# Kernel optimization log

Measured on AMD Instinct MI355X. Metric: run time of the kernel, lower is better.

The kernel has to match this reference:

```python
import jax, jax.numpy as jnp
import numpy as np

N = 27          # n_agents
NA = 33         # n_actions
OFF = 6         # semantic_action_offset
ATK = NA - OFF  # 27 attack actions
HID = 256       # rnn_hidden_dim
HEADS = 4
HD = 16         # head_dim
V = 8           # comm_value_dim
REL = 5
TOPK = 4
IN = 322
FLAT = HEADS * V  # 32
FUSE_SCALE = 0.1
GATE_FLOOR = 0.0
NEG = -1e10


def setup_inputs() -> dict:
    key = jax.random.key(0)
    ks = iter(jax.random.split(key, 40))
    r = lambda *s: jax.random.normal(next(ks), s, dtype=jnp.float32) * 0.05
    BS = 1024
    inp = {
        'inputs': jax.random.normal(next(ks), (BS * N, IN), dtype=jnp.float32),
        'hidden_state': jax.random.normal(next(ks), (BS * N, HID), dtype=jnp.float32),
        'relation_features': jax.random.normal(next(ks), (BS, N, N, REL), dtype=jnp.float32),
        'W1': r(HID, IN), 'b1': r(HID),
        'Wih': r(3 * HID, HID), 'bih': r(3 * HID),
        'Whh': r(3 * HID, HID), 'bhh': r(3 * HID),
        'Wp1': r(HID, HID), 'bp1': r(HID),
        'Wp2': r(NA, HID), 'bp2': r(NA),
        'Wq': r(HEADS * HD, HID), 'bq': r(HEADS * HD),
        'Wk': r(HEADS * HD, HID + REL), 'bk': r(HEADS * HD),
        'Wv': r(HEADS * V, ATK + 2), 'bv': r(HEADS * V),
        'ln_g': jnp.ones((FLAT,), jnp.float32), 'ln_b': jnp.zeros((FLAT,), jnp.float32),
        'Wg1': r(HID, HID + FLAT), 'bg1': r(HID),
        'Wg2': r(1, HID), 'bg2': jnp.full((1,), -2.5, jnp.float32),  # attack_gate_init_bias
        'Wd1': r(HID, HID + FLAT), 'bd1': r(HID),
        'Wd2': r(ATK, HID) * 0.2, 'bd2': r(ATK) * 0.2,  # small random instead of zero-init for nontrivial test
        'null_key': r(HEADS, HD), 'null_value': r(HEADS, V),
        'bs': BS,
    }
    return inp


def _topk_mask(scores, k):
    # scores: [bs, N, N+1, HEADS]; keep top-k along axis 2
    st = jnp.moveaxis(scores, 2, -1)                # [bs, N, HEADS, N+1]
    thr = jax.lax.top_k(st, k)[0][..., -1:]
    st = jnp.where(st >= thr, st, NEG)
    return jnp.moveaxis(st, -1, 2)


def _forward(inputs, hidden_state, relation_features, W1, b1, Wih, bih, Whh, bhh,
             Wp1, bp1, Wp2, bp2, Wq, bq, Wk, bk, Wv, bv, ln_g, ln_b,
             Wg1, bg1, Wg2, bg2, Wd1, bd1, Wd2, bd2, null_key, null_value, bs):
    x = jax.nn.relu(inputs @ W1.T + b1)
    h_in = hidden_state.reshape(-1, HID)
    # PyTorch GRUCell
    gi = x @ Wih.T + bih
    gh = h_in @ Whh.T + bhh
    ir, iz, inn = jnp.split(gi, 3, axis=-1)
    hr, hz, hn = jnp.split(gh, 3, axis=-1)
    rg = jax.nn.sigmoid(ir + hr)
    zg = jax.nn.sigmoid(iz + hz)
    ng = jnp.tanh(inn + rg * hn)
    h = (1.0 - zg) * ng + zg * h_in

    ah = h.reshape(bs, N, HID)                       # agent_hidden
    logits = jax.nn.relu(ah @ Wp1.T + bp1) @ Wp2.T + bp2   # [bs,N,NA]
    base_logits = logits[:, :, :OFF]
    attack_logits = logits[:, :, OFF:]

    # intent features (avail_actions=None path)
    attack_probs = jax.nn.softmax(attack_logits, axis=-1)
    top1 = jnp.max(attack_probs, axis=-1, keepdims=True)
    can_attack = jnp.ones((bs, N, 1), attack_probs.dtype)
    value_source = jnp.concatenate([attack_probs, can_attack, top1], axis=-1)
    sender_values = (value_source @ Wv.T + bv).reshape(bs, N, HEADS, V)

    queries = (ah @ Wq.T + bq).reshape(bs, N, HEADS, HD)
    # Linear over concat([sender_hidden, relation]) == split-weight sum
    Wk_h, Wk_r = Wk[:, :HID], Wk[:, HID:]
    key_h = ah @ Wk_h.T                              # [bs, N(send), A]
    key_r = jnp.einsum('bijr,ar->bija', relation_features, Wk_r)
    pair_keys = (key_h[:, None, :, :] + key_r + bk).reshape(bs, N, N, HEADS, HD)

    scale = 1.0 / np.sqrt(HD)
    scores = jnp.einsum('bihd,bijhd->bijh', queries, pair_keys) * scale
    eye = jnp.eye(N, dtype=bool)[None, :, :, None]
    scores = jnp.where(eye, NEG, scores)
    null_scores = jnp.einsum('bihd,hd->bih', queries, null_key)[:, :, None, :] * scale
    scores = jnp.concatenate([scores, null_scores], axis=2)   # [bs,N,N+1,HEADS]

    alpha = jax.nn.softmax(_topk_mask(scores, TOPK), axis=2)
    messages = (jnp.einsum('bijh,bjhv->bihv', alpha[:, :, :N], sender_values)
                + alpha[:, :, N, :, None] * null_value)        # [bs,N,HEADS,V]
    flat = messages.reshape(bs, N, FLAT)
    mu = jnp.mean(flat, axis=-1, keepdims=True)
    var = jnp.var(flat, axis=-1, keepdims=True)
    normed = (flat - mu) * jax.lax.rsqrt(var + 1e-5) * ln_g + ln_b

    fusion = jnp.concatenate([ah, normed], axis=-1)
    raw_gate = jax.nn.sigmoid(jax.nn.relu(fusion @ Wg1.T + bg1) @ Wg2.T + bg2)
    gate = GATE_FLOOR + (1.0 - GATE_FLOOR) * raw_gate
    delta = jax.nn.relu(fusion @ Wd1.T + bd1) @ Wd2.T + bd2
    fused = attack_logits + FUSE_SCALE * gate * delta
    final = jnp.concatenate([base_logits, fused], axis=-1).reshape(bs * N, NA)
    return final, h


def reference(inputs, hidden_state, relation_features, W1, b1, Wih, bih, Whh, bhh,
              Wp1, bp1, Wp2, bp2, Wq, bq, Wk, bk, Wv, bv, ln_g, ln_b,
              Wg1, bg1, Wg2, bg2, Wd1, bd1, Wd2, bd2, null_key, null_value, bs):
    return _forward(inputs, hidden_state, relation_features, W1, b1, Wih, bih, Whh, bhh,
                    Wp1, bp1, Wp2, bp2, Wq, bq, Wk, bk, Wv, bv, ln_g, ln_b,
                    Wg1, bg1, Wg2, bg2, Wd1, bd1, Wd2, bd2, null_key, null_value, bs)
```

## Files before the change

### kernel.cpp

```cpp
#include <hip/hip_runtime.h>
#include <cstdint>
#include <cstddef>

#define ROWS 27648
#define NEGV (-1e10f)

typedef __attribute__((ext_vector_type(8))) short bf16x8;
typedef __attribute__((ext_vector_type(4))) short short4v;
typedef __attribute__((ext_vector_type(4))) float f32x4;

__device__ __forceinline__ float sigmoidf_(float x) { return 1.f / (1.f + __expf(-x)); }
__device__ __forceinline__ float bf2f(short s) {
  union { float f; unsigned u; } x; x.u = ((unsigned)(unsigned short)s) << 16; return x.f;
}
__device__ __forceinline__ short f2bf(float f) {
  union { float f; unsigned u; } x; x.f = f;
  unsigned r = (x.u + 0x7fffu + ((x.u >> 16) & 1u)) >> 16;
  return (short)r;
}

#define GLDS(gp, lp) __builtin_amdgcn_global_load_lds( \
  (const __attribute__((address_space(1))) void*)(gp), \
  (__attribute__((address_space(3))) void*)(lp), 16, 0, 0)

template <int ACT, int BF16OUT>
__global__ __launch_bounds__(256) void gemm_mfma(
    const short* __restrict__ A, int lda,
    const short* __restrict__ B, int ldb,
    const float* __restrict__ bias,
    void* __restrict__ Cv, int ldc, int nstore, int K) {
  extern __shared__ short smem[];
  short* As = smem;
  short* Bs = smem + 8192;
  const int tid = threadIdx.x;
  const int wave = tid >> 6, lane = tid & 63;
  const int m0 = blockIdx.x * 128, n0 = blockIdx.y * 128;
  const int srow = lane >> 3;
  const int scol = ((lane & 7) ^ srow) * 8;
  const int sr0 = wave * 32;
  const int wm = (wave >> 1) * 64, wn = (wave & 1) * 64;
  const int fr = lane & 15, fk = (lane >> 4) * 8;

  f32x4 acc[4][4] = {};

  const short* pA = A + (size_t)(m0 + sr0 + srow) * lda + scol;
  const short* pB = B + (size_t)(n0 + sr0 + srow) * ldb + scol;
  short* lA = &As[sr0 * 64];
  short* lB = &Bs[sr0 * 64];

  const int KB = K & ~63;
  for (int k0 = 0; k0 < KB; k0 += 64) {
#pragma unroll
    for (int g = 0; g < 4; ++g) {
      GLDS(pA + k0 + g * 8 * lda, lA + g * 512);
      GLDS(pB + k0 + g * 8 * ldb, lB + g * 512);
    }
    __syncthreads();
#pragma unroll
    for (int ks = 0; ks < 2; ++ks) {
      bf16x8 af[4], bfr[4];
#pragma unroll
      for (int t = 0; t < 4; ++t) {
        const int ra = wm + t * 16 + fr;
        const int rb = wn + t * 16 + fr;
        af[t]  = *(const bf16x8*)&As[(ra * 64 + ks * 32 + fk) ^ ((ra & 7) << 3)];
        bfr[t] = *(const bf16x8*)&Bs[(rb * 64 + ks * 32 + fk) ^ ((rb & 7) << 3)];
      }
#pragma unroll
      for (int i = 0; i < 4; ++i)
#pragma unroll
        for (int j = 0; j < 4; ++j)
          acc[i][j] = __builtin_amdgcn_mfma_f32_16x16x32_bf16(af[i], bfr[j], acc[i][j], 0, 0, 0);
    }
    __syncthreads();
  }

  if (K & 32) {
    short* As2 = smem + 16384;
    short* Bs2 = smem + 20480;
    const int sr2 = lane >> 2, sc2 = (lane & 3) * 8;
    const short* qA = A + (size_t)(m0 + sr0 + sr2) * lda + sc2 + KB;
    const short* qB = B + (size_t)(n0 + sr0 + sr2) * ldb + sc2 + KB;
    GLDS(qA, &As2[sr0 * 32]);
    GLDS(qA + 16 * lda, &As2[(sr0 + 16) * 32]);
    GLDS(qB, &Bs2[sr0 * 32]);
    GLDS(qB + 16 * ldb, &Bs2[(sr0 + 16) * 32]);
    __syncthreads();
    bf16x8 af[4], bfr[4];
#pragma unroll
    for (int t = 0; t < 4; ++t) {
      af[t]  = *(const bf16x8*)&As2[(wm + t * 16 + fr) * 32 + fk];
      bfr[t] = *(const bf16x8*)&Bs2[(wn + t * 16 + fr) * 32 + fk];
    }
#pragma unroll
    for (int i = 0; i < 4; ++i)
#pragma unroll
      for (int j = 0; j < 4; ++j)
        acc[i][j] = __builtin_amdgcn_mfma_f32_16x16x32_bf16(af[i], bfr[j], acc[i][j], 0, 0, 0);
  }

  const int rbase = m0 + wm + (lane >> 4) * 4;
#pragma unroll
  for (int j = 0; j < 4; ++j) {
    const int col = n0 + wn + j * 16 + fr;
    if (col >= nstore) continue;
    const float bv = bias ? bias[col] : 0.f;
#pragma unroll
    for (int i = 0; i < 4; ++i)
#pragma unroll
      for (int r = 0; r < 4; ++r) {
        const int row = rbase + i * 16 + r;
        float v = acc[i][j][r] + bv;
        if (ACT) v = fmaxf(v, 0.f);
        if (BF16OUT) ((short*)Cv)[(size_t)row * ldc + col] = f2bf(v);
        else         ((float*)Cv)[(size_t)row * ldc + col] = v;
      }
  }
}

__global__ __launch_bounds__(256) void gemm_pqk(
    const short* __restrict__ A, const short* __restrict__ B,
    const float* __restrict__ bias,
    short* __restrict__ P1, float* __restrict__ QK) {
  extern __shared__ short smem[];
  short* As = smem;
  short* Bs = smem + 8192;
  const int tid = threadIdx.x;
  const int wave = tid >> 6, lane = tid & 63;
  const int m0 = blockIdx.x * 128, n0 = blockIdx.y * 128;
  const int srow = lane >> 3;
  const int scol = ((lane & 7) ^ srow) * 8;
  const int sr0 = wave * 32;
  const int wm = (wave >> 1) * 64, wn = (wave & 1) * 64;
  const int fr = lane & 15, fk = (lane >> 4) * 8;

  f32x4 acc[4][4] = {};
  const short* pA = A + (size_t)(m0 + sr0 + srow) * 288 + scol;
  const short* pB = B + (size_t)(n0 + sr0 + srow) * 256 + scol;
  short* lA = &As[sr0 * 64];
  short* lB = &Bs[sr0 * 64];

  for (int k0 = 0; k0 < 256; k0 += 64) {
#pragma unroll
    for (int g = 0; g < 4; ++g) {
      GLDS(pA + k0 + g * 8 * 288, lA + g * 512);
      GLDS(pB + k0 + g * 8 * 256, lB + g * 512);
    }
    __syncthreads();
#pragma unroll
    for (int ks = 0; ks < 2; ++ks) {
      bf16x8 af[4], bfr[4];
#pragma unroll
      for (int t = 0; t < 4; ++t) {
        const int ra = wm + t * 16 + fr;
        const int rb = wn + t * 16 + fr;
        af[t]  = *(const bf16x8*)&As[(ra * 64 + ks * 32 + fk) ^ ((ra & 7) << 3)];
        bfr[t] = *(const bf16x8*)&Bs[(rb * 64 + ks * 32 + fk) ^ ((rb & 7) << 3)];
      }
#pragma unroll
      for (int i = 0; i < 4; ++i)
#pragma unroll
        for (int j = 0; j < 4; ++j)
          acc[i][j] = __builtin_amdgcn_mfma_f32_16x16x32_bf16(af[i], bfr[j], acc[i][j], 0, 0, 0);
    }
    __syncthreads();
  }

  const int rbase = m0 + wm + (lane >> 4) * 4;
#pragma unroll
  for (int j = 0; j < 4; ++j) {
    const int col = n0 + wn + j * 16 + fr;
    if (col >= 384) continue;
    const float bv = bias[col];
#pragma unroll
    for (int i = 0; i < 4; ++i)
#pragma unroll
      for (int r = 0; r < 4; ++r) {
        const int row = rbase + i * 16 + r;
        float v = acc[i][j][r] + bv;
        if (col < 256) {
          P1[(size_t)row * 256 + col] = f2bf(fmaxf(v, 0.f));
        } else {
          QK[(size_t)row * 128 + (col - 256)] = v;
        }
      }
  }
}

__global__ __launch_bounds__(256) void conv_all(
    const float* __restrict__ inputs, const float* __restrict__ hidden,
    const float* __restrict__ W1, const float* __restrict__ Wih,
    const float* __restrict__ Whh, const float* __restrict__ Wp1,
    const float* __restrict__ Wp2, const float* __restrict__ Wq,
    const float* __restrict__ Wk, const float* __restrict__ Wg1,
    const float* __restrict__ Wd1, const float* __restrict__ Wg2,
    const float* __restrict__ Wd2, const float* __restrict__ bp1,
    const float* __restrict__ bq, const float* __restrict__ bg1,
    const float* __restrict__ bd1, const float* __restrict__ bg2,
    const float* __restrict__ bd2,
    short* __restrict__ xin, short* __restrict__ hid,
    short* __restrict__ w1w, short* __restrict__ wihw, short* __restrict__ whhw,
    short* __restrict__ wp2w, short* __restrict__ wpqk, short* __restrict__ wgdw,
    short* __restrict__ wfw, float* __restrict__ bpqkb, float* __restrict__ bgd,
    float* __restrict__ bf2v) {
  const int NX = ROWS * 352;
  const int NH = ROWS * 256;
  int idx = blockIdx.x * 256 + threadIdx.x;
  if (idx < NX) {
    int row = idx / 352, c = idx - row * 352;
    xin[idx] = (c < 322) ? f2bf(inputs[row * 322 + c]) : (short)0;
    return;
  }
  idx -= NX;
  if (idx < NH) { hid[idx] = f2bf(hidden[idx]); return; }
  idx -= NH;
  if (idx < 90112) {
    int r = idx / 352, c = idx - r * 352;
    w1w[idx] = (c < 322) ? f2bf(W1[r * 322 + c]) : (short)0;
    return;
  }
  idx -= 90112;
  if (idx < 196608) { wihw[idx] = f2bf(Wih[idx]); return; }
  idx -= 196608;
  if (idx < 196608) { whhw[idx] = f2bf(Whh[idx]); return; }
  idx -= 196608;
  if (idx < 32768) {
    wp2w[idx] = (idx < 33 * 256) ? f2bf(Wp2[idx]) : (short)0;
    return;
  }
  idx -= 32768;
  if (idx < 131072) {
    int r = idx >> 8, c = idx & 255;
    short v = 0;
    if (r < 256) v = f2bf(Wp1[r * 256 + c]);
    else if (r < 320) v = f2bf(Wq[(r - 256) * 256 + c]);
    else if (r < 384) v = f2bf(Wk[(size_t)(r - 320) * 261 + c]);
    wpqk[idx] = v;
    return;
  }
  idx -= 131072;
  if (idx < 147456) {
    wgdw[idx] = (idx < 73728) ? f2bf(Wg1[idx]) : f2bf(Wd1[idx - 73728]);
    return;
  }
  idx -= 147456;
  if (idx < 65536) {
    int r = idx >> 9, c = idx & 511;
    short v = 0;
    if (r == 0 && c < 256) v = f2bf(Wg2[c]);
    else if (r >= 1 && r < 28 && c >= 256) v = f2bf(Wd2[(r - 1) * 256 + (c - 256)]);
    wfw[idx] = v;
    return;
  }
  idx -= 65536;
  if (idx < 384) {
    bpqkb[idx] = (idx < 256) ? bp1[idx] : ((idx < 320) ? bq[idx - 256] : 0.f);
    return;
  }
  idx -= 384;
  if (idx < 512) { bgd[idx] = (idx < 256) ? bg1[idx] : bd1[idx - 256]; return; }
  idx -= 512;
  if (idx < 128)
    bf2v[idx] = (idx == 0) ? bg2[0] : ((idx < 28) ? bd2[idx - 1] : 0.f);
}

__global__ __launch_bounds__(256) void gru_kernel(
    const short* __restrict__ GI, const short* __restrict__ GH,
    const float* __restrict__ Hin, float* __restrict__ H,
    short* __restrict__ FUS) {
  int idx = blockIdx.x * 256 + threadIdx.x;
  int row = idx >> 6;
  int c = (idx & 63) * 4;
  const short4v gr = *(const short4v*)(GI + (size_t)row * 768 + c);
  const short4v gz = *(const short4v*)(GI + (size_t)row * 768 + 256 + c);
  const short4v gn = *(const short4v*)(GI + (size_t)row * 768 + 512 + c);
  const short4v hr = *(const short4v*)(GH + (size_t)row * 768 + c);
  const short4v hz = *(const short4v*)(GH + (size_t)row * 768 + 256 + c);
  const short4v hn = *(const short4v*)(GH + (size_t)row * 768 + 512 + c);
  const f32x4 hi = *(const f32x4*)(Hin + (size_t)row * 256 + c);
  f32x4 o;
  short4v ob;
#pragma unroll
  for (int p = 0; p < 4; ++p) {
    float r = sigmoidf_(bf2f(gr[p]) + bf2f(hr[p]));
    float z = sigmoidf_(bf2f(gz[p]) + bf2f(hz[p]));
    float n = tanhf(bf2f(gn[p]) + r * bf2f(hn[p]));
    float h = (1.f - z) * n + z * hi[p];
    o[p] = h;
    ob[p] = f2bf(h);
  }
  *(f32x4*)(H + (size_t)row * 256 + c) = o;
  *(short4v*)(FUS + (size_t)row * 288 + c) = ob;
}

__global__ __launch_bounds__(256) void sv_kernel(
    const float* __restrict__ logits, const float* __restrict__ Wv,
    const float* __restrict__ bv, float* __restrict__ SV) {
  const int wave = threadIdx.x >> 6;
  const int lane = threadIdx.x & 63;
  const int row = blockIdx.x * 4 + wave;
  __shared__ float vs_s[4][29];
  float v = (lane < 27) ? logits[(size_t)row * 33 + 6 + lane] : -INFINITY;
  float m = v;
#pragma unroll
  for (int off = 32; off; off >>= 1) m = fmaxf(m, __shfl_xor(m, off));
  float e = (lane < 27) ? __expf(v - m) : 0.f;
  float s = e;
#pragma unroll
  for (int off = 32; off; off >>= 1) s += __shfl_xor(s, off);
  if (lane < 27) vs_s[wave][lane] = e / s;
  if (lane == 27) vs_s[wave][27] = 1.f;
  if (lane == 28) vs_s[wave][28] = 1.f / s;
  __syncthreads();
  if (lane < 32) {
    float acc = bv[lane];
    const float* w = Wv + lane * 29;
#pragma unroll
    for (int c = 0; c < 29; ++c) acc += w[c] * vs_s[wave][c];
    SV[(size_t)row * 32 + lane] = acc;
  }
}

__global__ __launch_bounds__(256) void attn4_kernel(
    const float* __restrict__ QK, const float* __restrict__ rel,
    const float* __restrict__ Wk, const float* __restrict__ bk,
    const float* __restrict__ SV, const float* __restrict__ null_key,
    const float* __restrict__ null_value, const float* __restrict__ ln_g,
    const float* __restrict__ ln_b, short* __restrict__ FUS) {
  const int b  = blockIdx.x;
  const int iq = blockIdx.y;
  const int t = threadIdx.x;
  const int wave = t >> 6, lane = t & 63;
  const int i = iq * 4 + wave;
  const int iw = (i < 27) ? i : 26;

  __shared__ float kh_s[64 * 29];
  __shared__ float sv_s[28 * 32];
  __shared__ float q_s[4][64];
  __shared__ float wkr_s[320];
  __shared__ float bk_s[64], nk_s[64];
  __shared__ float lng_s[32], lnb_s[32];
  __shared__ float rel_s[4][136];
  __shared__ float qws[4][28];
  __shared__ float s_row[4][112];

  for (int idx = t; idx < 27 * 64; idx += 256) {
    int r = idx >> 6, c = idx & 63;
    kh_s[c * 29 + r] = QK[(size_t)(b * 27 + r) * 128 + 64 + c];
  }
  for (int idx = t; idx < 27 * 32; idx += 256)
    sv_s[idx] = SV[(size_t)b * 864 + idx];
  q_s[wave][lane] = QK[(size_t)(b * 27 + iw) * 128 + lane];
  for (int idx = t; idx < 320; idx += 256) {
    int a = idx / 5, r = idx - a * 5;
    wkr_s[idx] = Wk[(size_t)a * 261 + 256 + r];
  }
  if (t < 64) bk_s[t] = bk[t];
  else if (t < 128) nk_s[t - 64] = null_key[t - 64];
  else if (t < 160) sv_s[27 * 32 + (t - 128)] = null_value[t - 128];
  else if (t < 192) { lng_s[t - 160] = ln_g[t - 160]; lnb_s[t - 160] = ln_b[t - 160]; }
  for (int idx = lane; idx < 135; idx += 64)
    rel_s[wave][idx] = rel[(size_t)(b * 27 + iw) * 135 + idx];
  __syncthreads();

  if (lane < 28) {
    float acc = 0.f;
    if (lane < 20) {
      const int h = lane / 5, r = lane - h * 5;
#pragma unroll
      for (int d = 0; d < 16; ++d)
        acc += q_s[wave][h * 16 + d] * wkr_s[(h * 16 + d) * 5 + r];
    } else if (lane < 24) {
      const int h = lane - 20;
#pragma unroll
      for (int d = 0; d < 16; ++d)
        acc += q_s[wave][h * 16 + d] * bk_s[h * 16 + d];
    } else {
      const int h = lane - 24;
#pragma unroll
      for (int d = 0; d < 16; ++d)
        acc += q_s[wave][h * 16 + d] * nk_s[h * 16 + d];
    }
    qws[wave][lane] = acc;
  }
  __builtin_amdgcn_wave_barrier();

#pragma unroll
  for (int pass = 0; pass < 2; ++pass) {
    const int item = pass * 64 + lane;
    if (item < 112) {
      const int j = item >> 2, h = item & 3;
      float s;
      if (j < 27) {
        float acc = qws[wave][20 + h];
        const float* q  = &q_s[wave][h * 16];
        const float* kh = &kh_s[(h * 16) * 29 + j];
#pragma unroll
        for (int d = 0; d < 16; ++d) acc += q[d] * kh[d * 29];
        const float* rp = &rel_s[wave][j * 5];
        const float* qw = &qws[wave][h * 5];
#pragma unroll
        for (int r = 0; r < 5; ++r) acc += rp[r] * qw[r];
        s = acc * 0.25f;
        if (j == i) s = NEGV;
      } else {
        s = qws[wave][24 + h] * 0.25f;
      }
      s_row[wave][item] = s;
    }
  }
  __builtin_amdgcn_wave_barrier();

  {
    const int g = lane >> 4;
    const int li = lane & 15;
    const int j1 = li + 16;
    const float v0 = s_row[wave][li * 4 + g];
    const float v1 = (j1 < 28) ? s_row[wave][j1 * 4 + g] : -INFINITY;
    float w0 = v0, w1 = v1;
    float m0 = 0.f, thr = 0.f;
#pragma unroll
    for (int r = 0; r < 4; ++r) {
      float gm = fmaxf(w0, w1);
#pragma unroll
      for (int off = 8; off; off >>= 1) gm = fmaxf(gm, __shfl_xor(gm, off));
      if (r == 0) m0 = gm;
      thr = gm;
      const unsigned long long b0 = __ballot(w0 == gm);
      const unsigned long long b1 = __ballot(w1 == gm);
      const unsigned seg0 = (unsigned)(b0 >> (g * 16)) & 0xFFFFu;
      const unsigned seg1 = (unsigned)(b1 >> (g * 16)) & 0xFFFFu;
      if (seg0) { if (li == __builtin_ctz(seg0)) w0 = -INFINITY; }
      else      { if (li == __builtin_ctz(seg1)) w1 = -INFINITY; }
    }
    float e0 = (v0 >= thr) ? __expf(v0 - m0) : 0.f;
    float e1 = (j1 < 28 && v1 >= thr) ? __expf(v1 - m0) : 0.f;
    float s = e0 + e1;
#pragma unroll
    for (int off = 8; off; off >>= 1) s += __shfl_xor(s, off);
    const float inv = 1.f / s;
    s_row[wave][li * 4 + g] = e0 * inv;
    if (j1 < 28) s_row[wave][j1 * 4 + g] = e1 * inv;
  }
  __builtin_amdgcn_wave_barrier();

  {
    const int sl = lane & 31;
    const int h = sl >> 3;
    const int jbase = (lane >> 5) * 14;
    const float* al = &s_row[wave][h];
    float acc = 0.f;
#pragma unroll
    for (int jj = 0; jj < 14; ++jj)
      acc += al[(jbase + jj) * 4] * sv_s[(jbase + jj) * 32 + sl];
    acc += __shfl_xor(acc, 32);
    float sum = acc;
#pragma unroll
    for (int off = 16; off; off >>= 1) sum += __shfl_xor(sum, off);
    const float mu = sum * (1.f / 32.f);
    const float d = acc - mu;
    float sq = d * d;
#pragma unroll
    for (int off = 16; off; off >>= 1) sq += __shfl_xor(sq, off);
    const float rs = rsqrtf(sq * (1.f / 32.f) + 1e-5f);
    const float nv = d * rs * lng_s[sl] + lnb_s[sl];
    if (i < 27 && lane < 32)
      FUS[(size_t)(b * 27 + i) * 288 + 256 + sl] = f2bf(nv);
  }
}

__global__ __launch_bounds__(256) void fuse_kernel(
    const float* __restrict__ GDf, const float* __restrict__ LOG,
    float* __restrict__ out) {
  int idx = blockIdx.x * 256 + threadIdx.x;
  int row = idx / 33, c = idx - row * 33;
  float v = LOG[idx];
  if (c >= 6) {
    float gate = sigmoidf_(GDf[(size_t)row * 28]);
    v += 0.1f * gate * GDf[(size_t)row * 28 + (c - 5)];
  }
  out[idx] = v;
}

extern "C" void kernel_launch(void* const* d_in, const int* in_sizes, int n_in,
                              void* d_out, int out_size, void* d_ws, size_t ws_size,
                              hipStream_t stream) {
  const float* inputs = (const float*)d_in[0];
  const float* hidden = (const float*)d_in[1];
  const float* rel    = (const float*)d_in[2];
  const float* W1  = (const float*)d_in[3];  const float* b1  = (const float*)d_in[4];
  const float* Wih = (const float*)d_in[5];  const float* bih = (const float*)d_in[6];
  const float* Whh = (const float*)d_in[7];  const float* bhh = (const float*)d_in[8];
  const float* Wp1 = (const float*)d_in[9];  const float* bp1 = (const float*)d_in[10];
  const float* Wp2 = (const float*)d_in[11]; const float* bp2 = (const float*)d_in[12];
  const float* Wq  = (const float*)d_in[13]; const float* bq  = (const float*)d_in[14];
  const float* Wk  = (const float*)d_in[15]; const float* bk  = (const float*)d_in[16];
  const float* Wv  = (const float*)d_in[17]; const float* bv  = (const float*)d_in[18];
  const float* ln_g = (const float*)d_in[19]; const float* ln_b = (const float*)d_in[20];
  const float* Wg1 = (const float*)d_in[21]; const float* bg1 = (const float*)d_in[22];
  const float* Wg2 = (const float*)d_in[23]; const float* bg2 = (const float*)d_in[24];
  const float* Wd1 = (const float*)d_in[25]; const float* bd1 = (const float*)d_in[26];
  const float* Wd2 = (const float*)d_in[27]; const float* bd2 = (const float*)d_in[28];
  const float* null_key   = (const float*)d_in[29];
  const float* null_value = (const float*)d_in[30];

  char* wsb = (char*)d_ws;
  short* GIB = (short*)(wsb + 0);
  short* GDB = (short*)(wsb + 0);
  short* XINB = (short*)(wsb + 42467328);
  short* GHB  = (short*)(wsb + 42467328);
  float* LOG  = (float*)(wsb + 42467328);
  float* QKB  = (float*)(wsb + 42467328 + 4194304);
  float* SVB  = (float*)(wsb + 42467328 + 18874368);
  float* LOGD = (float*)(wsb + 42467328 + 23068672);
  short* XB   = (short*)(wsb + 84934656);
  short* FUS  = (short*)(wsb + 84934656);
  short* HIDB = (short*)(wsb + 84934656 + 16777216);
  short* P1B  = (short*)(wsb + 84934656 + 16777216);
  char* wb = wsb + 115867648;
  short* W1W   = (short*)(wb + 0);
  short* WIHW  = (short*)(wb + 180224);
  short* WHHW  = (short*)(wb + 573440);
  short* WP2W  = (short*)(wb + 966656);
  short* WPQK  = (short*)(wb + 1032192);
  short* WGDW  = (short*)(wb + 1294336);
  short* WFW   = (short*)(wb + 1589248);
  float* BPQKb = (float*)(wb + 1720320);
  float* BGD   = (float*)(wb + 1721856);
  float* BF2   = (float*)(wb + 1723904);

  float* out = (float*)d_out;
  float* H   = out + (size_t)ROWS * 33;

  conv_all<<<69028, 256, 0, stream>>>(inputs, hidden,
                                      W1, Wih, Whh, Wp1, Wp2, Wq, Wk, Wg1, Wd1,
                                      Wg2, Wd2, bp1, bq, bg1, bd1, bg2, bd2,
                                      XINB, HIDB,
                                      W1W, WIHW, WHHW, WP2W, WPQK, WGDW, WFW,
                                      BPQKb, BGD, BF2);
  gemm_mfma<1, 1><<<dim3(216, 2), 256, 49152, stream>>>(XINB, 352, W1W, 352, b1, XB, 256, 256, 352);
  gemm_mfma<0, 1><<<dim3(216, 6), 256, 32768, stream>>>(XB, 256, WIHW, 256, bih, GIB, 768, 768, 256);
  gemm_mfma<0, 1><<<dim3(216, 6), 256, 32768, stream>>>(HIDB, 256, WHHW, 256, bhh, GHB, 768, 768, 256);
  gru_kernel<<<6912, 256, 0, stream>>>(GIB, GHB, hidden, H, FUS);
  gemm_pqk<<<dim3(216, 3), 256, 32768, stream>>>(FUS, WPQK, BPQKb, P1B, QKB);
  gemm_mfma<0, 0><<<dim3(216, 1), 256, 32768, stream>>>(P1B, 256, WP2W, 256, bp2, LOG, 33, 33, 256);
  sv_kernel<<<6912, 256, 0, stream>>>(LOG, Wv, bv, SVB);
  attn4_kernel<<<dim3(1024, 7), 256, 0, stream>>>(QKB, rel, Wk, bk, SVB, null_key,
                                                  null_value, ln_g, ln_b, FUS);
  gemm_mfma<1, 1><<<dim3(216, 4), 256, 49152, stream>>>(FUS, 288, WGDW, 288, BGD, GDB, 512, 512, 288);
  gemm_mfma<0, 0><<<dim3(216, 1), 256, 32768, stream>>>(GDB, 512, WFW, 512, BF2, LOGD, 28, 28, 512);
  fuse_kernel<<<3564, 256, 0, stream>>>(LOGD, LOG, out);
}
```

Before: 404.5 us.

## Process two query rows per wave in attention kernel to cut block count

The attention kernel now has each wave handle two query agents (i and i+16), so the grid shrinks from 7 to 4 blocks per batch. The per-batch key and value staging into shared memory is therefore repeated fewer times across blocks. Query vectors and per-head projections are held in registers, and relation features are read straight from global memory instead of being staged in shared memory. The cost is more registers per thread and duplicated reductions, with some wasted lanes for the last partial row group.

```diff
diff --git a/kernel.cpp b/kernel.cpp
--- a/kernel.cpp
+++ b/kernel.cpp
@@ -321,28 +321,29 @@
   }
 }
 
-__global__ __launch_bounds__(256) void attn4_kernel(
+__global__ __launch_bounds__(256) void attn7_kernel(
     const float* __restrict__ QK, const float* __restrict__ rel,
     const float* __restrict__ Wk, const float* __restrict__ bk,
     const float* __restrict__ SV, const float* __restrict__ null_key,
     const float* __restrict__ null_value, const float* __restrict__ ln_g,
     const float* __restrict__ ln_b, short* __restrict__ FUS) {
-  const int b  = blockIdx.x;
-  const int iq = blockIdx.y;
+  const int b = blockIdx.x;
+  const int y = blockIdx.y;
   const int t = threadIdx.x;
   const int wave = t >> 6, lane = t & 63;
-  const int i = iq * 4 + wave;
-  const int iw = (i < 27) ? i : 26;
+  const int iA = y * 4 + wave;
+  const int iB = iA + 16;
+  const int bBv = (iB < 27);
+  const int iBw = bBv ? iB : 26;
 
   __shared__ float kh_s[64 * 29];
   __shared__ float sv_s[28 * 32];
-  __shared__ float q_s[4][64];
   __shared__ float wkr_s[320];
   __shared__ float bk_s[64], nk_s[64];
   __shared__ float lng_s[32], lnb_s[32];
-  __shared__ float rel_s[4][136];
-  __shared__ float qws[4][28];
-  __shared__ float s_row[4][112];
+  __shared__ float q_s[4][2][64];
+  __shared__ float qws_s[4][2][28];
+  __shared__ float s_row[4][2][112];
 
   for (int idx = t; idx < 27 * 64; idx += 256) {
     int r = idx >> 6, c = idx & 63;
@@ -350,7 +351,6 @@
   }
   for (int idx = t; idx < 27 * 32; idx += 256)
     sv_s[idx] = SV[(size_t)b * 864 + idx];
-  q_s[wave][lane] = QK[(size_t)(b * 27 + iw) * 128 + lane];
   for (int idx = t; idx < 320; idx += 256) {
     int a = idx / 5, r = idx - a * 5;
     wkr_s[idx] = Wk[(size_t)a * 261 + 256 + r];
@@ -359,54 +359,75 @@
   else if (t < 128) nk_s[t - 64] = null_key[t - 64];
   else if (t < 160) sv_s[27 * 32 + (t - 128)] = null_value[t - 128];
   else if (t < 192) { lng_s[t - 160] = ln_g[t - 160]; lnb_s[t - 160] = ln_b[t - 160]; }
-  for (int idx = lane; idx < 135; idx += 64)
-    rel_s[wave][idx] = rel[(size_t)(b * 27 + iw) * 135 + idx];
+  q_s[wave][0][lane] = QK[(size_t)(b * 27 + iA) * 128 + lane];
+  q_s[wave][1][lane] = QK[(size_t)(b * 27 + iBw) * 128 + lane];
   __syncthreads();
 
-  if (lane < 28) {
-    float acc = 0.f;
-    if (lane < 20) {
-      const int h = lane / 5, r = lane - h * 5;
-#pragma unroll
-      for (int d = 0; d < 16; ++d)
-        acc += q_s[wave][h * 16 + d] * wkr_s[(h * 16 + d) * 5 + r];
-    } else if (lane < 24) {
-      const int h = lane - 20;
-#pragma unroll
-      for (int d = 0; d < 16; ++d)
-        acc += q_s[wave][h * 16 + d] * bk_s[h * 16 + d];
-    } else {
-      const int h = lane - 24;
-#pragma unroll
-      for (int d = 0; d < 16; ++d)
-        acc += q_s[wave][h * 16 + d] * nk_s[h * 16 + d];
-    }
-    qws[wave][lane] = acc;
+  {
+    const int s = lane >> 5;
+    const int ls = lane & 31;
+    if (ls < 28) {
+      float acc = 0.f;
+      const float* q = q_s[wave][s];
+      if (ls < 20) {
+        const int qh = ls / 5, r = ls - qh * 5;
+#pragma unroll
+        for (int d = 0; d < 16; ++d)
+          acc += q[qh * 16 + d] * wkr_s[(qh * 16 + d) * 5 + r];
+      } else if (ls < 24) {
+        const int qh = ls - 20;
+#pragma unroll
+        for (int d = 0; d < 16; ++d)
+          acc += q[qh * 16 + d] * bk_s[qh * 16 + d];
+      } else {
+        const int qh = ls - 24;
+#pragma unroll
+        for (int d = 0; d < 16; ++d)
+          acc += q[qh * 16 + d] * nk_s[qh * 16 + d];
+      }
+      qws_s[wave][s][ls] = acc;
+    }
   }
   __builtin_amdgcn_wave_barrier();
 
-#pragma unroll
-  for (int pass = 0; pass < 2; ++pass) {
-    const int item = pass * 64 + lane;
+  const int h = lane & 3;
+  float qw[2][5], qbk[2], qnull[2];
+  f32x4 qreg[2][4];
+#pragma unroll
+  for (int s = 0; s < 2; ++s) {
+#pragma unroll
+    for (int r = 0; r < 5; ++r) qw[s][r] = qws_s[wave][s][h * 5 + r];
+    qbk[s]   = qws_s[wave][s][20 + h];
+    qnull[s] = qws_s[wave][s][24 + h];
+#pragma unroll
+    for (int c = 0; c < 4; ++c)
+      qreg[s][c] = *(const f32x4*)&q_s[wave][s][h * 16 + c * 4];
+  }
+  const float* relA = rel + (size_t)(b * 27 + iA) * 135;
+  const float* relB = rel + (size_t)(b * 27 + iBw) * 135;
+
+#pragma unroll
+  for (int p = 0; p < 4; ++p) {
+    const int item = (p & 1) * 64 + lane;
+    const int s = p >> 1;
     if (item < 112) {
-      const int j = item >> 2, h = item & 3;
-      float s;
+      const int j = item >> 2;
+      float sc;
       if (j < 27) {
-        float acc = qws[wave][20 + h];
-        const float* q  = &q_s[wave][h * 16];
+        float acc = qbk[s];
         const float* kh = &kh_s[(h * 16) * 29 + j];
 #pragma unroll
-        for (int d = 0; d < 16; ++d) acc += q[d] * kh[d * 29];
-        const float* rp = &rel_s[wave][j * 5];
-        const float* qw = &qws[wave][h * 5];
-#pragma unroll
-        for (int r = 0; r < 5; ++r) acc += rp[r] * qw[r];
-        s = acc * 0.25f;
-        if (j == i) s = NEGV;
+        for (int d = 0; d < 16; ++d) acc += qreg[s][d >> 2][d & 3] * kh[d * 29];
+        const float* rp = (s ? relB : relA) + j * 5;
+        acc += rp[0] * qw[s][0] + rp[1] * qw[s][1] + rp[2] * qw[s][2]
+             + rp[3] * qw[s][3] + rp[4] * qw[s][4];
+        sc = acc * 0.25f;
+        const int ii = s ? iB : iA;
+        if (j == ii) sc = NEGV;
       } else {
-        s = qws[wave][24 + h] * 0.25f;
-      }
-      s_row[wave][item] = s;
+        sc = qnull[s] * 0.25f;
+      }
+      s_row[wave][s][item] = sc;
     }
   }
   __builtin_amdgcn_wave_barrier();
@@ -414,58 +435,95 @@
   {
     const int g = lane >> 4;
     const int li = lane & 15;
-    const int j1 = li + 16;
-    const float v0 = s_row[wave][li * 4 + g];
-    const float v1 = (j1 < 28) ? s_row[wave][j1 * 4 + g] : -INFINITY;
-    float w0 = v0, w1 = v1;
-    float m0 = 0.f, thr = 0.f;
+    const int jj1 = li + 16;
+    float v0[2], v1[2], w0[2], w1[2], m0[2], thr[2];
+#pragma unroll
+    for (int s = 0; s < 2; ++s) {
+      v0[s] = s_row[wave][s][li * 4 + g];
+      v1[s] = (jj1 < 28) ? s_row[wave][s][jj1 * 4 + g] : -INFINITY;
+      w0[s] = v0[s]; w1[s] = v1[s];
+    }
 #pragma unroll
     for (int r = 0; r < 4; ++r) {
-      float gm = fmaxf(w0, w1);
-#pragma unroll
-      for (int off = 8; off; off >>= 1) gm = fmaxf(gm, __shfl_xor(gm, off));
-      if (r == 0) m0 = gm;
-      thr = gm;
-      const unsigned long long b0 = __ballot(w0 == gm);
-      const unsigned long long b1 = __ballot(w1 == gm);
-      const unsigned seg0 = (unsigned)(b0 >> (g * 16)) & 0xFFFFu;
-      const unsigned seg1 = (unsigned)(b1 >> (g * 16)) & 0xFFFFu;
-      if (seg0) { if (li == __builtin_ctz(seg0)) w0 = -INFINITY; }
-      else      { if (li == __builtin_ctz(seg1)) w1 = -INFINITY; }
-    }
-    float e0 = (v0 >= thr) ? __expf(v0 - m0) : 0.f;
-    float e1 = (j1 < 28 && v1 >= thr) ? __expf(v1 - m0) : 0.f;
-    float s = e0 + e1;
-#pragma unroll
-    for (int off = 8; off; off >>= 1) s += __shfl_xor(s, off);
-    const float inv = 1.f / s;
-    s_row[wave][li * 4 + g] = e0 * inv;
-    if (j1 < 28) s_row[wave][j1 * 4 + g] = e1 * inv;
+      float gm[2];
+#pragma unroll
+      for (int s = 0; s < 2; ++s) gm[s] = fmaxf(w0[s], w1[s]);
+#pragma unroll
+      for (int off = 8; off; off >>= 1) {
+#pragma unroll
+        for (int s = 0; s < 2; ++s) gm[s] = fmaxf(gm[s], __shfl_xor(gm[s], off));
+      }
+#pragma unroll
+      for (int s = 0; s < 2; ++s) {
+        if (r == 0) m0[s] = gm[s];
+        thr[s] = gm[s];
+        const unsigned long long b0 = __ballot(w0[s] == gm[s]);
+        const unsigned long long b1 = __ballot(w1[s] == gm[s]);
+        const unsigned seg0 = (unsigned)(b0 >> (g * 16)) & 0xFFFFu;
+        const unsigned seg1 = (unsigned)(b1 >> (g * 16)) & 0xFFFFu;
+        if (seg0) { if (li == __builtin_ctz(seg0)) w0[s] = -INFINITY; }
+        else      { if (li == __builtin_ctz(seg1)) w1[s] = -INFINITY; }
+      }
+    }
+    float e0[2], e1[2], inv[2];
+#pragma unroll
+    for (int s = 0; s < 2; ++s) {
+      e0[s] = (v0[s] >= thr[s]) ? __expf(v0[s] - m0[s]) : 0.f;
+      e1[s] = (jj1 < 28 && v1[s] >= thr[s]) ? __expf(v1[s] - m0[s]) : 0.f;
+    }
+    float ssum[2];
+#pragma unroll
+    for (int s = 0; s < 2; ++s) ssum[s] = e0[s] + e1[s];
+#pragma unroll
+    for (int off = 8; off; off >>= 1) {
+#pragma unroll
+      for (int s = 0; s < 2; ++s) ssum[s] += __shfl_xor(ssum[s], off);
+    }
+#pragma unroll
+    for (int s = 0; s < 2; ++s) {
+      inv[s] = 1.f / ssum[s];
+      s_row[wave][s][li * 4 + g] = e0[s] * inv[s];
+      if (jj1 < 28) s_row[wave][s][jj1 * 4 + g] = e1[s] * inv[s];
+    }
   }
   __builtin_amdgcn_wave_barrier();
 
   {
     const int sl = lane & 31;
-    const int h = sl >> 3;
+    const int mh = sl >> 3;
     const int jbase = (lane >> 5) * 14;
-    const float* al = &s_row[wave][h];
-    float acc = 0.f;
-#pragma unroll
-    for (int jj = 0; jj < 14; ++jj)
-      acc += al[(jbase + jj) * 4] * sv_s[(jbase + jj) * 32 + sl];
-    acc += __shfl_xor(acc, 32);
-    float sum = acc;
-#pragma unroll
-    for (int off = 16; off; off >>= 1) sum += __shfl_xor(sum, off);
-    const float mu = sum * (1.f / 32.f);
-    const float d = acc - mu;
-    float sq = d * d;
-#pragma unroll
-    for (int off = 16; off; off >>= 1) sq += __shfl_xor(sq, off);
-    const float rs = rsqrtf(sq * (1.f / 32.f) + 1e-5f);
-    const float nv = d * rs * lng_s[sl] + lnb_s[sl];
-    if (i < 27 && lane < 32)
-      FUS[(size_t)(b * 27 + i) * 288 + 256 + sl] = f2bf(nv);
+    float acc[2] = {0.f, 0.f};
+#pragma unroll
+    for (int jj = 0; jj < 14; ++jj) {
+      const int j = jbase + jj;
+      const float svv = sv_s[j * 32 + sl];
+      acc[0] += s_row[wave][0][j * 4 + mh] * svv;
+      acc[1] += s_row[wave][1][j * 4 + mh] * svv;
+    }
+#pragma unroll
+    for (int s = 0; s < 2; ++s) acc[s] += __shfl_xor(acc[s], 32);
+    float sum[2] = {acc[0], acc[1]};
+#pragma unroll
+    for (int off = 16; off; off >>= 1) {
+#pragma unroll
+      for (int s = 0; s < 2; ++s) sum[s] += __shfl_xor(sum[s], off);
+    }
+    float d[2], sq[2];
+#pragma unroll
+    for (int s = 0; s < 2; ++s) { d[s] = acc[s] - sum[s] * (1.f / 32.f); sq[s] = d[s] * d[s]; }
+#pragma unroll
+    for (int off = 16; off; off >>= 1) {
+#pragma unroll
+      for (int s = 0; s < 2; ++s) sq[s] += __shfl_xor(sq[s], off);
+    }
+    if (lane < 32) {
+      const float nvA = d[0] * rsqrtf(sq[0] * (1.f / 32.f) + 1e-5f) * lng_s[sl] + lnb_s[sl];
+      FUS[(size_t)(b * 27 + iA) * 288 + 256 + sl] = f2bf(nvA);
+      if (bBv) {
+        const float nvB = d[1] * rsqrtf(sq[1] * (1.f / 32.f) + 1e-5f) * lng_s[sl] + lnb_s[sl];
+        FUS[(size_t)(b * 27 + iB) * 288 + 256 + sl] = f2bf(nvB);
+      }
+    }
   }
 }
 
@@ -545,7 +603,7 @@
   gemm_pqk<<<dim3(216, 3), 256, 32768, stream>>>(FUS, WPQK, BPQKb, P1B, QKB);
   gemm_mfma<0, 0><<<dim3(216, 1), 256, 32768, stream>>>(P1B, 256, WP2W, 256, bp2, LOG, 33, 33, 256);
   sv_kernel<<<6912, 256, 0, stream>>>(LOG, Wv, bv, SVB);
-  attn4_kernel<<<dim3(1024, 7), 256, 0, stream>>>(QKB, rel, Wk, bk, SVB, null_key,
+  attn7_kernel<<<dim3(1024, 4), 256, 0, stream>>>(QKB, rel, Wk, bk, SVB, null_key,
                                                   null_value, ln_g, ln_b, FUS);
   gemm_mfma<1, 1><<<dim3(216, 4), 256, 49152, stream>>>(FUS, 288, WGDW, 288, BGD, GDB, 512, 512, 288);
   gemm_mfma<0, 0><<<dim3(216, 1), 256, 32768, stream>>>(GDB, 512, WFW, 512, BF2, LOGD, 28, 28, 512);
```

Measured after the change: 397.5 us. No clear change (-1.7%).
